# Kernel optimization log

Hardware: AMD Instinct MI355X
Metric: run time of the kernel (lower is better)

## Reference

```python
import jax, jax.numpy as jnp
import numpy as np

K = 4          # knn (loop=True -> self included as nearest)
NEG_SLOPE = 0.2  # PyG GATConv leaky_relu slope


def knn_neighbors(coords, k=K):
    """coords: [B, P, 2] -> global neighbor indices [B*P, k].
    Per-batch brute-force kNN (cdist + top_k), sequential over batch to
    bound the [P, P] distance matrix memory, matching torch_cluster.knn_graph
    with loop=True and a per-image batch vector."""
    B, P, _ = coords.shape

    def per_batch(c):  # c: [P, 2]
        d = jnp.sum((c[:, None, :] - c[None, :, :]) ** 2, axis=-1)  # [P, P]
        _, idx = jax.lax.top_k(-d, k)  # self (dist 0) is included -> loop=True
        return idx

    idx = jax.lax.map(per_batch, coords)  # [B, P, k], local indices
    offs = (jnp.arange(B, dtype=idx.dtype) * P)[:, None, None]
    return (idx + offs).reshape(B * P, k)  # global node ids


def gat_layer(x, nbr, W, a_src, a_dst, b, concat):
    """PyG GATConv (eval mode, dropout off) on a fixed-degree kNN graph.
    x: [N, Cin], nbr: [N, k] source nodes j for each target i.
    alpha_ij = softmax_j leaky_relu(a_src.h_j + a_dst.h_i); out_i = sum_j alpha_ij h_j."""
    H, F = a_src.shape
    h = (x @ W).reshape(-1, H, F)                      # [N, H, F]
    asrc = jnp.einsum('nhf,hf->nh', h, a_src)          # [N, H]
    adst = jnp.einsum('nhf,hf->nh', h, a_dst)          # [N, H]
    e = jax.nn.leaky_relu(asrc[nbr] + adst[:, None, :], NEG_SLOPE)  # [N, k, H]
    alpha = jax.nn.softmax(e, axis=1)                  # softmax over neighbors
    out = jnp.einsum('nkh,nkhf->nhf', alpha, h[nbr])   # [N, H, F]
    if concat:
        out = out.reshape(-1, H * F)
    else:
        out = out.mean(axis=1)                         # heads=1 -> identity
    return out + b


def gat_forward(coords, x, W0, att_src0, att_dst0, b0, W1, att_src1, att_dst1, b1,
                W2, att_src2, att_dst2, b2):
    B, P, _ = coords.shape
    nbr = knn_neighbors(coords)
    h = gat_layer(x, nbr, W0, att_src0, att_dst0, b0, concat=True)
    h = jax.nn.elu(h)
    h = gat_layer(h, nbr, W1, att_src1, att_dst1, b1, concat=True)
    h = jax.nn.elu(h)
    h = gat_layer(h, nbr, W2, att_src2, att_dst2, b2, concat=False)
    return h.reshape(B, P, -1)  # pred_logits [B, P, num_classes+1]


def setup_inputs() -> dict:
    key = jax.random.key(0)
    ks = jax.random.split(key, 16)
    B, P, N = 16, 8192, 16 * 8192
    s = 0.05
    return {
        'coords': jax.random.uniform(ks[0], (B, P, 2), dtype=jnp.float32),
        'x': jax.random.normal(ks[1], (N, 256), dtype=jnp.float32),
        'W0': jax.random.normal(ks[2], (256, 256), dtype=jnp.float32) * s,
        'att_src0': jax.random.normal(ks[3], (4, 64), dtype=jnp.float32) * s,
        'att_dst0': jax.random.normal(ks[4], (4, 64), dtype=jnp.float32) * s,
        'b0': jax.random.normal(ks[5], (256,), dtype=jnp.float32) * s,
        'W1': jax.random.normal(ks[6], (256, 256), dtype=jnp.float32) * s,
        'att_src1': jax.random.normal(ks[7], (4, 64), dtype=jnp.float32) * s,
        'att_dst1': jax.random.normal(ks[8], (4, 64), dtype=jnp.float32) * s,
        'b1': jax.random.normal(ks[9], (256,), dtype=jnp.float32) * s,
        'W2': jax.random.normal(ks[10], (256, 2), dtype=jnp.float32) * s,
        'att_src2': jax.random.normal(ks[11], (1, 2), dtype=jnp.float32) * s,
        'att_dst2': jax.random.normal(ks[12], (1, 2), dtype=jnp.float32) * s,
        'b2': jax.random.normal(ks[13], (2,), dtype=jnp.float32) * s,
    }


def reference(coords, x, W0, att_src0, att_dst0, b0, W1, att_src1, att_dst1, b1,
              W2, att_src2, att_dst2, b2):
    return gat_forward(coords, x, W0, att_src0, att_dst0, b0,
                       W1, att_src1, att_dst1, b1, W2, att_src2, att_dst2, b2)
```

## Files before the change

### kernel.cpp

```cpp
#include <hip/hip_runtime.h>
#include <math.h>

constexpr int Bn = 16, Pn = 8192, Nn = 16 * 8192;
constexpr int GB = 32;
constexpr int NBIN = GB * GB;

typedef __attribute__((ext_vector_type(8))) short short8;
typedef __attribute__((ext_vector_type(4))) float f32x4;

__device__ __forceinline__ unsigned short f2bf(float f) {
  unsigned u = __builtin_bit_cast(unsigned, f);
  unsigned r = (u + 0x7FFFu + ((u >> 16) & 1u)) >> 16;
  return (unsigned short)r;
}
__device__ __forceinline__ float bf2f(unsigned short h) {
  unsigned u = ((unsigned)h) << 16;
  return __builtin_bit_cast(float, u);
}

__global__ __launch_bounds__(256) void bin_count(const float* __restrict__ coords,
                                                 int* __restrict__ counts) {
  const int n = blockIdx.x * 256 + threadIdx.x;
  const int b = n >> 13;
  float2 c = ((const float2*)coords)[n];
  int bx = min(GB - 1, (int)(c.x * (float)GB));
  int by = min(GB - 1, (int)(c.y * (float)GB));
  atomicAdd(&counts[b * NBIN + by * GB + bx], 1);
}

__global__ __launch_bounds__(1024) void bin_scan(const int* __restrict__ counts,
                                                 int* __restrict__ starts,
                                                 int* __restrict__ cursor) {
  __shared__ int s[NBIN];
  const int b = blockIdx.x, t = threadIdx.x;
  const int v = counts[b * NBIN + t];
  s[t] = v;
  __syncthreads();
  for (int off = 1; off < NBIN; off <<= 1) {
    int x = (t >= off) ? s[t - off] : 0;
    __syncthreads();
    s[t] += x;
    __syncthreads();
  }
  const int excl = s[t] - v;
  starts[b * NBIN + t] = excl;
  cursor[b * NBIN + t] = excl;
}

__global__ __launch_bounds__(256) void bin_scatter(const float* __restrict__ coords,
                                                   int* __restrict__ cursor,
                                                   float2* __restrict__ pts,
                                                   int* __restrict__ ids) {
  const int n = blockIdx.x * 256 + threadIdx.x;
  const int b = n >> 13, p = n & (Pn - 1);
  float2 c = ((const float2*)coords)[n];
  int bx = min(GB - 1, (int)(c.x * (float)GB));
  int by = min(GB - 1, (int)(c.y * (float)GB));
  int slot = atomicAdd(&cursor[b * NBIN + by * GB + bx], 1);
  pts[(size_t)b * Pn + slot] = c;
  ids[(size_t)b * Pn + slot] = p;
}

__global__ __launch_bounds__(256) void knn_query(const float* __restrict__ coords,
                                                 const int* __restrict__ starts,
                                                 const int* __restrict__ counts,
                                                 const float2* __restrict__ pts,
                                                 const int* __restrict__ ids,
                                                 int* __restrict__ nbr) {
  const int n = blockIdx.x * 256 + threadIdx.x;
  const int b = n >> 13;
  const float2 q = ((const float2*)coords)[n];
  const float qx = q.x, qy = q.y;
  const float w = 1.0f / (float)GB;
  const int bx = min(GB - 1, (int)(qx * (float)GB));
  const int by = min(GB - 1, (int)(qy * (float)GB));
  const float2* bp = pts + (size_t)b * Pn;
  const int* bi = ids + (size_t)b * Pn;
  const int* bs = starts + b * NBIN;
  const int* bc = counts + b * NBIN;

  float d0v = 3.4e38f, d1v = 3.4e38f, d2v = 3.4e38f, d3v = 3.4e38f;
  int i0v = 0x7fffffff, i1v = 0x7fffffff, i2v = 0x7fffffff, i3v = 0x7fffffff;

#define LLT(da, ia, db, ib) ((da) < (db) || ((da) == (db) && (ia) < (ib)))
#define LEX_INSERT(dd, jj)                                              \
  if (LLT(dd, jj, d3v, i3v)) {                                          \
    if (LLT(dd, jj, d2v, i2v)) {                                        \
      d3v = d2v; i3v = i2v;                                             \
      if (LLT(dd, jj, d1v, i1v)) {                                      \
        d2v = d1v; i2v = i1v;                                           \
        if (LLT(dd, jj, d0v, i0v)) { d1v = d0v; i1v = i0v; d0v = dd; i0v = jj; } \
        else { d1v = dd; i1v = jj; }                                    \
      } else { d2v = dd; i2v = jj; }                                    \
    } else { d3v = dd; i3v = jj; }                                      \
  }
#define SCAN_CELL(xx, yy)                                               \
  {                                                                     \
    const int cell = (yy) * GB + (xx);                                  \
    const int s0 = bs[cell], cnt = bc[cell];                            \
    for (int s = s0; s < s0 + cnt; ++s) {                               \
      float2 pp = bp[s];                                                \
      int jj = bi[s];                                                   \
      float dx = qx - pp.x, dy = qy - pp.y;                             \
      float dd = __fadd_rn(__fmul_rn(dx, dx), __fmul_rn(dy, dy));       \
      LEX_INSERT(dd, jj);                                               \
    }                                                                   \
  }

  for (int k = 0; k < GB; ++k) {
    const int xlo = bx - k, xhi = bx + k, ylo = by - k, yhi = by + k;
    const int cxlo = max(0, xlo), cxhi = min(GB - 1, xhi);
    const int cylo = max(0, ylo), cyhi = min(GB - 1, yhi);
    for (int yy = cylo; yy <= cyhi; ++yy) {
      const bool edge = (yy == ylo) || (yy == yhi);
      if (edge || k == 0) {
        for (int xx = cxlo; xx <= cxhi; ++xx) SCAN_CELL(xx, yy);
      } else {
        if (xlo >= 0) SCAN_CELL(xlo, yy);
        if (xhi <= GB - 1) SCAN_CELL(xhi, yy);
      }
    }
    float m = 1e30f;
    bool open = false;
    if (xlo > 0)      { m = fminf(m, qx - (float)xlo * w); open = true; }
    if (xhi < GB - 1) { m = fminf(m, (float)(xhi + 1) * w - qx); open = true; }
    if (ylo > 0)      { m = fminf(m, qy - (float)ylo * w); open = true; }
    if (yhi < GB - 1) { m = fminf(m, (float)(yhi + 1) * w - qy); open = true; }
    if (!open) break;
    m -= 1e-6f;
    if (d3v < 3.0e38f && m > 0.f && __fmul_rn(m, m) >= d3v) break;
  }
#undef SCAN_CELL
#undef LEX_INSERT
#undef LLT

  const int base = b * Pn;
  *(int4*)&nbr[(size_t)n * 4] =
      make_int4(base + i0v, base + i1v, base + i2v, base + i3v);
}

__global__ __launch_bounds__(256) void wt_kernel(const float* __restrict__ W,
                                                 unsigned short* __restrict__ Wth,
                                                 unsigned short* __restrict__ Wtl) {
  const int k = blockIdx.x, n = threadIdx.x;
  float v = W[k * 256 + n];
  unsigned short h = f2bf(v);
  unsigned short l = f2bf(v - bf2f(h));
  Wth[n * 256 + k] = h;
  Wtl[n * 256 + k] = l;
}

__global__ __launch_bounds__(256, 3) void gemm_bf3(const float* __restrict__ A,
                                                   const unsigned short* __restrict__ Bth,
                                                   const unsigned short* __restrict__ Btl,
                                                   const float* __restrict__ att_src,
                                                   const float* __restrict__ att_dst,
                                                   float* __restrict__ C,
                                                   float* __restrict__ asrc,
                                                   float* __restrict__ adst) {
  __shared__ unsigned short Ah[128][36], Al[128][36];
  __shared__ unsigned short Bh[128][36], Bl[128][36];
  const int t = threadIdx.x;
  const int row0 = blockIdx.y * 128;
  const int col0 = blockIdx.x * 128;
  const int wid = t >> 6, lane = t & 63;
  const int wr = (wid >> 1) * 64, wc = (wid & 1) * 64;
  const int lrow = lane & 15, lko = (lane >> 4) * 8;

  f32x4 acc[4][4];
#pragma unroll
  for (int i = 0; i < 4; ++i)
#pragma unroll
    for (int j = 0; j < 4; ++j) acc[i][j] = {0.f, 0.f, 0.f, 0.f};

  float4 av[4];
  uint4 bhv[2], blv[2];

#define GLOAD(ktv)                                                          \
  {                                                                         \
    const int k0 = (ktv) * 32;                                              \
    _Pragma("unroll")                                                       \
    for (int i = 0; i < 4; ++i) {                                           \
      const int idx = t + i * 256;                                          \
      const int row = idx >> 3, kq = idx & 7;                               \
      av[i] = *(const float4*)&A[(size_t)(row0 + row) * 256 + k0 + kq * 4]; \
    }                                                                       \
    _Pragma("unroll")                                                       \
    for (int i = 0; i < 2; ++i) {                                           \
      const int idx = t + i * 256;                                          \
      const int col = idx >> 2, kc = idx & 3;                               \
      bhv[i] = *(const uint4*)&Bth[(size_t)(col0 + col) * 256 + k0 + kc * 8]; \
      blv[i] = *(const uint4*)&Btl[(size_t)(col0 + col) * 256 + k0 + kc * 8]; \
    }                                                                       \
  }

  GLOAD(0);
  for (int kt = 0; kt < 8; ++kt) {
    __syncthreads();
#pragma unroll
    for (int i = 0; i < 4; ++i) {
      const int idx = t + i * 256;
      const int row = idx >> 3, kq = idx & 7;
      const float vv[4] = {av[i].x, av[i].y, av[i].z, av[i].w};
      unsigned short hh[4], ll[4];
#pragma unroll
      for (int e = 0; e < 4; ++e) {
        hh[e] = f2bf(vv[e]);
        ll[e] = f2bf(vv[e] - bf2f(hh[e]));
      }
      *(ushort4*)&Ah[row][kq * 4] = make_ushort4(hh[0], hh[1], hh[2], hh[3]);
      *(ushort4*)&Al[row][kq * 4] = make_ushort4(ll[0], ll[1], ll[2], ll[3]);
    }
#pragma unroll
    for (int i = 0; i < 2; ++i) {
      const int idx = t + i * 256;
      const int col = idx >> 2, kc = idx & 3;
      *(uint4*)&Bh[col][kc * 8] = bhv[i];
      *(uint4*)&Bl[col][kc * 8] = blv[i];
    }
    __syncthreads();
    if (kt < 7) GLOAD(kt + 1);
    short8 afh[4], afl[4], bfh[4], bfl[4];
#pragma unroll
    for (int f = 0; f < 4; ++f) {
      afh[f] = *(const short8*)&Ah[wr + f * 16 + lrow][lko];
      afl[f] = *(const short8*)&Al[wr + f * 16 + lrow][lko];
      bfh[f] = *(const short8*)&Bh[wc + f * 16 + lrow][lko];
      bfl[f] = *(const short8*)&Bl[wc + f * 16 + lrow][lko];
    }
#pragma unroll
    for (int fr = 0; fr < 4; ++fr)
#pragma unroll
      for (int fc = 0; fc < 4; ++fc) {
        acc[fr][fc] = __builtin_amdgcn_mfma_f32_16x16x32_bf16(afh[fr], bfh[fc], acc[fr][fc], 0, 0, 0);
        acc[fr][fc] = __builtin_amdgcn_mfma_f32_16x16x32_bf16(afh[fr], bfl[fc], acc[fr][fc], 0, 0, 0);
        acc[fr][fc] = __builtin_amdgcn_mfma_f32_16x16x32_bf16(afl[fr], bfh[fc], acc[fr][fc], 0, 0, 0);
      }
  }
#undef GLOAD

#pragma unroll
  for (int fr = 0; fr < 4; ++fr)
#pragma unroll
    for (int fc = 0; fc < 4; ++fc) {
      const int col = col0 + wc + fc * 16 + lrow;
#pragma unroll
      for (int j = 0; j < 4; ++j) {
        const int row = row0 + wr + fr * 16 + (lane >> 4) * 4 + j;
        C[(size_t)row * 256 + col] = acc[fr][fc][j];
      }
    }

  const int h = (col0 >> 6) + (wid & 1);
  float asv[4], adv[4];
#pragma unroll
  for (int fc = 0; fc < 4; ++fc) {
    asv[fc] = att_src[h * 64 + fc * 16 + lrow];
    adv[fc] = att_dst[h * 64 + fc * 16 + lrow];
  }
#pragma unroll
  for (int fr = 0; fr < 4; ++fr)
#pragma unroll
    for (int j = 0; j < 4; ++j) {
      float ps = 0.f, pd = 0.f;
#pragma unroll
      for (int fc = 0; fc < 4; ++fc) {
        ps += acc[fr][fc][j] * asv[fc];
        pd += acc[fr][fc][j] * adv[fc];
      }
#pragma unroll
      for (int off = 1; off < 16; off <<= 1) {
        ps += __shfl_xor(ps, off);
        pd += __shfl_xor(pd, off);
      }
      if (lrow == 0) {
        const int row = row0 + wr + fr * 16 + (lane >> 4) * 4 + j;
        asrc[(size_t)row * 4 + h] = ps;
        adst[(size_t)row * 4 + h] = pd;
      }
    }
}

__device__ __forceinline__ float leaky02(float x) { return x >= 0.f ? x : 0.2f * x; }

__global__ __launch_bounds__(256) void aggregate_fused(const float* __restrict__ g,
                                                       const int* __restrict__ nbr,
                                                       const float* __restrict__ asrc,
                                                       const float* __restrict__ adst,
                                                       const float* __restrict__ bias,
                                                       float* __restrict__ y) {
  const int t = threadIdx.x;
  const int lane = t & 63;
  const int n = blockIdx.x * 4 + (t >> 6);
  int4 nb = *(const int4*)&nbr[(size_t)n * 4];
  const int h = lane >> 4;
  const float adh = adst[(size_t)n * 4 + h];
  float e0 = leaky02(asrc[(size_t)nb.x * 4 + h] + adh);
  float e1 = leaky02(asrc[(size_t)nb.y * 4 + h] + adh);
  float e2 = leaky02(asrc[(size_t)nb.z * 4 + h] + adh);
  float e3 = leaky02(asrc[(size_t)nb.w * 4 + h] + adh);
  float m = fmaxf(fmaxf(fmaxf(e0, e1), e2), e3);
  float x0 = expf(e0 - m), x1 = expf(e1 - m), x2 = expf(e2 - m), x3 = expf(e3 - m);
  float s = ((x0 + x1) + x2) + x3;
  const float a0 = x0 / s, a1 = x1 / s, a2 = x2 / s, a3 = x3 / s;

  const int c = lane * 4;
  float4 v0 = *(const float4*)&g[(size_t)nb.x * 256 + c];
  float4 v1 = *(const float4*)&g[(size_t)nb.y * 256 + c];
  float4 v2 = *(const float4*)&g[(size_t)nb.z * 256 + c];
  float4 v3 = *(const float4*)&g[(size_t)nb.w * 256 + c];
  float4 bb = *(const float4*)&bias[c];
  float4 o;
  o.x = a0 * v0.x + a1 * v1.x + a2 * v2.x + a3 * v3.x + bb.x;
  o.y = a0 * v0.y + a1 * v1.y + a2 * v2.y + a3 * v3.y + bb.y;
  o.z = a0 * v0.z + a1 * v1.z + a2 * v2.z + a3 * v3.z + bb.z;
  o.w = a0 * v0.w + a1 * v1.w + a2 * v2.w + a3 * v3.w + bb.w;
  o.x = o.x > 0.f ? o.x : expm1f(o.x);
  o.y = o.y > 0.f ? o.y : expm1f(o.y);
  o.z = o.z > 0.f ? o.z : expm1f(o.z);
  o.w = o.w > 0.f ? o.w : expm1f(o.w);
  *(float4*)&y[(size_t)n * 256 + c] = o;
}

__global__ __launch_bounds__(256) void aggregate_h2(const float* __restrict__ g,
                                                    const int* __restrict__ nbr,
                                                    const float* __restrict__ asrc,
                                                    const float* __restrict__ adst,
                                                    const float* __restrict__ bias,
                                                    const float* __restrict__ W2,
                                                    const float* __restrict__ as2,
                                                    const float* __restrict__ ad2,
                                                    float* __restrict__ g2,
                                                    float* __restrict__ asrc2,
                                                    float* __restrict__ adst2) {
  const int t = threadIdx.x;
  const int lane = t & 63;
  const int n = blockIdx.x * 4 + (t >> 6);
  int4 nb = *(const int4*)&nbr[(size_t)n * 4];
  const int h = lane >> 4;
  const float adh = adst[(size_t)n * 4 + h];
  float e0 = leaky02(asrc[(size_t)nb.x * 4 + h] + adh);
  float e1 = leaky02(asrc[(size_t)nb.y * 4 + h] + adh);
  float e2 = leaky02(asrc[(size_t)nb.z * 4 + h] + adh);
  float e3 = leaky02(asrc[(size_t)nb.w * 4 + h] + adh);
  float m = fmaxf(fmaxf(fmaxf(e0, e1), e2), e3);
  float x0 = expf(e0 - m), x1 = expf(e1 - m), x2 = expf(e2 - m), x3 = expf(e3 - m);
  float s = ((x0 + x1) + x2) + x3;
  const float a0 = x0 / s, a1 = x1 / s, a2 = x2 / s, a3 = x3 / s;

  const int c = lane * 4;
  float4 v0 = *(const float4*)&g[(size_t)nb.x * 256 + c];
  float4 v1 = *(const float4*)&g[(size_t)nb.y * 256 + c];
  float4 v2 = *(const float4*)&g[(size_t)nb.z * 256 + c];
  float4 v3 = *(const float4*)&g[(size_t)nb.w * 256 + c];
  float4 bb = *(const float4*)&bias[c];
  float4 o;
  o.x = a0 * v0.x + a1 * v1.x + a2 * v2.x + a3 * v3.x + bb.x;
  o.y = a0 * v0.y + a1 * v1.y + a2 * v2.y + a3 * v3.y + bb.y;
  o.z = a0 * v0.z + a1 * v1.z + a2 * v2.z + a3 * v3.z + bb.z;
  o.w = a0 * v0.w + a1 * v1.w + a2 * v2.w + a3 * v3.w + bb.w;
  o.x = o.x > 0.f ? o.x : expm1f(o.x);
  o.y = o.y > 0.f ? o.y : expm1f(o.y);
  o.z = o.z > 0.f ? o.z : expm1f(o.z);
  o.w = o.w > 0.f ? o.w : expm1f(o.w);

  const float w00 = W2[(c + 0) * 2 + 0], w01 = W2[(c + 0) * 2 + 1];
  const float w10 = W2[(c + 1) * 2 + 0], w11 = W2[(c + 1) * 2 + 1];
  const float w20 = W2[(c + 2) * 2 + 0], w21 = W2[(c + 2) * 2 + 1];
  const float w30 = W2[(c + 3) * 2 + 0], w31 = W2[(c + 3) * 2 + 1];
  float p0 = o.x * w00 + o.y * w10 + o.z * w20 + o.w * w30;
  float p1 = o.x * w01 + o.y * w11 + o.z * w21 + o.w * w31;
#pragma unroll
  for (int off = 1; off < 64; off <<= 1) {
    p0 += __shfl_xor(p0, off);
    p1 += __shfl_xor(p1, off);
  }
  if (lane == 0) {
    g2[(size_t)n * 2]     = p0;
    g2[(size_t)n * 2 + 1] = p1;
    asrc2[n] = p0 * as2[0] + p1 * as2[1];
    adst2[n] = p0 * ad2[0] + p1 * ad2[1];
  }
}

__global__ __launch_bounds__(256) void final_kernel(const int* __restrict__ nbr,
                                                    const float* __restrict__ g2,
                                                    const float* __restrict__ asrc2,
                                                    const float* __restrict__ adst2,
                                                    const float* __restrict__ b2,
                                                    float* __restrict__ out) {
  const int n = blockIdx.x * 256 + threadIdx.x;
  int4 nb = *(const int4*)&nbr[(size_t)n * 4];
  const float ad = adst2[n];
  float e0 = leaky02(asrc2[nb.x] + ad);
  float e1 = leaky02(asrc2[nb.y] + ad);
  float e2 = leaky02(asrc2[nb.z] + ad);
  float e3 = leaky02(asrc2[nb.w] + ad);
  float m = fmaxf(fmaxf(e0, e1), fmaxf(e2, e3));
  float x0 = expf(e0 - m), x1 = expf(e1 - m), x2 = expf(e2 - m), x3 = expf(e3 - m);
  float s = x0 + x1 + x2 + x3;
  float o0 = (x0 * g2[(size_t)nb.x * 2] + x1 * g2[(size_t)nb.y * 2] +
              x2 * g2[(size_t)nb.z * 2] + x3 * g2[(size_t)nb.w * 2]) / s;
  float o1 = (x0 * g2[(size_t)nb.x * 2 + 1] + x1 * g2[(size_t)nb.y * 2 + 1] +
              x2 * g2[(size_t)nb.z * 2 + 1] + x3 * g2[(size_t)nb.w * 2 + 1]) / s;
  out[(size_t)n * 2]     = o0 + b2[0];
  out[(size_t)n * 2 + 1] = o1 + b2[1];
}

extern "C" void kernel_launch(void* const* d_in, const int* in_sizes, int n_in,
                              void* d_out, int out_size, void* d_ws, size_t ws_size,
                              hipStream_t stream) {
  const float* coords = (const float*)d_in[0];
  const float* x   = (const float*)d_in[1];
  const float* W0  = (const float*)d_in[2];
  const float* as0 = (const float*)d_in[3];
  const float* ad0 = (const float*)d_in[4];
  const float* b0  = (const float*)d_in[5];
  const float* W1  = (const float*)d_in[6];
  const float* as1 = (const float*)d_in[7];
  const float* ad1 = (const float*)d_in[8];
  const float* b1  = (const float*)d_in[9];
  const float* W2  = (const float*)d_in[10];
  const float* as2 = (const float*)d_in[11];
  const float* ad2 = (const float*)d_in[12];
  const float* b2  = (const float*)d_in[13];
  float* out = (float*)d_out;

  float* g     = (float*)d_ws;
  float* y     = g + (size_t)Nn * 256;
  int*   nbr   = (int*)(y + (size_t)Nn * 256);
  float* asrc  = (float*)(nbr + (size_t)Nn * 4);
  float* adst  = asrc + (size_t)Nn * 4;
  float* g2    = adst + (size_t)Nn * 4;
  float* s2    = g2 + (size_t)Nn * 2;
  float* d2    = s2 + (size_t)Nn;
  unsigned short* Wth = (unsigned short*)(d2 + (size_t)Nn);
  unsigned short* Wtl = Wth + 256 * 256;
  float2* pts  = (float2*)(Wtl + 256 * 256);
  int* ids     = (int*)(pts + (size_t)Bn * Pn);
  int* counts  = ids + (size_t)Bn * Pn;
  int* starts  = counts + Bn * NBIN;
  int* cursor  = starts + Bn * NBIN;

  hipMemsetAsync(counts, 0, Bn * NBIN * sizeof(int), stream);
  bin_count<<<Nn / 256, 256, 0, stream>>>(coords, counts);
  bin_scan<<<Bn, NBIN, 0, stream>>>(counts, starts, cursor);
  bin_scatter<<<Nn / 256, 256, 0, stream>>>(coords, cursor, pts, ids);
  knn_query<<<Nn / 256, 256, 0, stream>>>(coords, starts, counts, pts, ids, nbr);

  wt_kernel<<<256, 256, 0, stream>>>(W0, Wth, Wtl);
  gemm_bf3<<<dim3(2, Nn / 128), 256, 0, stream>>>(x, Wth, Wtl, as0, ad0, g, asrc, adst);
  aggregate_fused<<<Nn / 4, 256, 0, stream>>>(g, nbr, asrc, adst, b0, y);

  wt_kernel<<<256, 256, 0, stream>>>(W1, Wth, Wtl);
  gemm_bf3<<<dim3(2, Nn / 128), 256, 0, stream>>>(y, Wth, Wtl, as1, ad1, g, asrc, adst);
  aggregate_h2<<<Nn / 4, 256, 0, stream>>>(g, nbr, asrc, adst, b1, W2, as2, ad2,
                                           g2, s2, d2);

  final_kernel<<<Nn / 256, 256, 0, stream>>>(nbr, g2, s2, d2, b2, out);
}
```

Before: 706.7 us.

## Load GEMM B fragments directly from global and swap MFMA operands for vector stores

The pre-split bf16 weight fragments are now read straight from global memory (L2/L1-resident) into registers instead of being staged through shared memory. This halves the LDS footprint and the LDS traffic per k-step. The MFMA operands are swapped so each lane holds 4 consecutive output columns, which allows float4 stores of C and an attention-logit reduction needing only two cross-lane shuffles instead of four. The cost is more global load instructions per wave, each issued right before its use with little latency hiding.

```diff
diff --git a/kernel.cpp b/kernel.cpp
--- a/kernel.cpp
+++ b/kernel.cpp
@@ -159,13 +159,13 @@
                                                    float* __restrict__ asrc,
                                                    float* __restrict__ adst) {
   __shared__ unsigned short Ah[128][36], Al[128][36];
-  __shared__ unsigned short Bh[128][36], Bl[128][36];
   const int t = threadIdx.x;
   const int row0 = blockIdx.y * 128;
   const int col0 = blockIdx.x * 128;
   const int wid = t >> 6, lane = t & 63;
   const int wr = (wid >> 1) * 64, wc = (wid & 1) * 64;
   const int lrow = lane & 15, lko = (lane >> 4) * 8;
+  const int cg = (lane >> 4) * 4;
 
   f32x4 acc[4][4];
 #pragma unroll
@@ -174,7 +174,6 @@
     for (int j = 0; j < 4; ++j) acc[i][j] = {0.f, 0.f, 0.f, 0.f};
 
   float4 av[4];
-  uint4 bhv[2], blv[2];
 
 #define GLOAD(ktv)                                                          \
   {                                                                         \
@@ -185,13 +184,6 @@
       const int row = idx >> 3, kq = idx & 7;                               \
       av[i] = *(const float4*)&A[(size_t)(row0 + row) * 256 + k0 + kq * 4]; \
     }                                                                       \
-    _Pragma("unroll")                                                       \
-    for (int i = 0; i < 2; ++i) {                                           \
-      const int idx = t + i * 256;                                          \
-      const int col = idx >> 2, kc = idx & 3;                               \
-      bhv[i] = *(const uint4*)&Bth[(size_t)(col0 + col) * 256 + k0 + kc * 8]; \
-      blv[i] = *(const uint4*)&Btl[(size_t)(col0 + col) * 256 + k0 + kc * 8]; \
-    }                                                                       \
   }
 
   GLOAD(0);
@@ -211,74 +203,68 @@
       *(ushort4*)&Ah[row][kq * 4] = make_ushort4(hh[0], hh[1], hh[2], hh[3]);
       *(ushort4*)&Al[row][kq * 4] = make_ushort4(ll[0], ll[1], ll[2], ll[3]);
     }
-#pragma unroll
-    for (int i = 0; i < 2; ++i) {
-      const int idx = t + i * 256;
-      const int col = idx >> 2, kc = idx & 3;
-      *(uint4*)&Bh[col][kc * 8] = bhv[i];
-      *(uint4*)&Bl[col][kc * 8] = blv[i];
-    }
     __syncthreads();
     if (kt < 7) GLOAD(kt + 1);
-    short8 afh[4], afl[4], bfh[4], bfl[4];
+
+    short8 bfh[4], bfl[4];
+#pragma unroll
+    for (int f = 0; f < 4; ++f) {
+      const size_t boff = (size_t)(col0 + wc + f * 16 + lrow) * 256 + kt * 32 + lko;
+      bfh[f] = *(const short8*)&Bth[boff];
+      bfl[f] = *(const short8*)&Btl[boff];
+    }
+    short8 afh[4], afl[4];
 #pragma unroll
     for (int f = 0; f < 4; ++f) {
       afh[f] = *(const short8*)&Ah[wr + f * 16 + lrow][lko];
       afl[f] = *(const short8*)&Al[wr + f * 16 + lrow][lko];
-      bfh[f] = *(const short8*)&Bh[wc + f * 16 + lrow][lko];
-      bfl[f] = *(const short8*)&Bl[wc + f * 16 + lrow][lko];
     }
 #pragma unroll
     for (int fr = 0; fr < 4; ++fr)
 #pragma unroll
       for (int fc = 0; fc < 4; ++fc) {
-        acc[fr][fc] = __builtin_amdgcn_mfma_f32_16x16x32_bf16(afh[fr], bfh[fc], acc[fr][fc], 0, 0, 0);
-        acc[fr][fc] = __builtin_amdgcn_mfma_f32_16x16x32_bf16(afh[fr], bfl[fc], acc[fr][fc], 0, 0, 0);
-        acc[fr][fc] = __builtin_amdgcn_mfma_f32_16x16x32_bf16(afl[fr], bfh[fc], acc[fr][fc], 0, 0, 0);
+        acc[fr][fc] = __builtin_amdgcn_mfma_f32_16x16x32_bf16(bfh[fc], afh[fr], acc[fr][fc], 0, 0, 0);
+        acc[fr][fc] = __builtin_amdgcn_mfma_f32_16x16x32_bf16(bfl[fc], afh[fr], acc[fr][fc], 0, 0, 0);
+        acc[fr][fc] = __builtin_amdgcn_mfma_f32_16x16x32_bf16(bfh[fc], afl[fr], acc[fr][fc], 0, 0, 0);
       }
   }
 #undef GLOAD
 
 #pragma unroll
-  for (int fr = 0; fr < 4; ++fr)
+  for (int fr = 0; fr < 4; ++fr) {
+    const int row = row0 + wr + fr * 16 + lrow;
 #pragma unroll
     for (int fc = 0; fc < 4; ++fc) {
-      const int col = col0 + wc + fc * 16 + lrow;
-#pragma unroll
-      for (int j = 0; j < 4; ++j) {
-        const int row = row0 + wr + fr * 16 + (lane >> 4) * 4 + j;
-        C[(size_t)row * 256 + col] = acc[fr][fc][j];
-      }
-    }
+      const int col = col0 + wc + fc * 16 + cg;
+      *(f32x4*)&C[(size_t)row * 256 + col] = acc[fr][fc];
+    }
+  }
 
   const int h = (col0 >> 6) + (wid & 1);
-  float asv[4], adv[4];
+  float4 asv[4], adv[4];
 #pragma unroll
   for (int fc = 0; fc < 4; ++fc) {
-    asv[fc] = att_src[h * 64 + fc * 16 + lrow];
-    adv[fc] = att_dst[h * 64 + fc * 16 + lrow];
-  }
-#pragma unroll
-  for (int fr = 0; fr < 4; ++fr)
-#pragma unroll
-    for (int j = 0; j < 4; ++j) {
-      float ps = 0.f, pd = 0.f;
-#pragma unroll
-      for (int fc = 0; fc < 4; ++fc) {
-        ps += acc[fr][fc][j] * asv[fc];
-        pd += acc[fr][fc][j] * adv[fc];
-      }
-#pragma unroll
-      for (int off = 1; off < 16; off <<= 1) {
-        ps += __shfl_xor(ps, off);
-        pd += __shfl_xor(pd, off);
-      }
-      if (lrow == 0) {
-        const int row = row0 + wr + fr * 16 + (lane >> 4) * 4 + j;
-        asrc[(size_t)row * 4 + h] = ps;
-        adst[(size_t)row * 4 + h] = pd;
-      }
-    }
+    asv[fc] = *(const float4*)&att_src[h * 64 + fc * 16 + cg];
+    adv[fc] = *(const float4*)&att_dst[h * 64 + fc * 16 + cg];
+  }
+#pragma unroll
+  for (int fr = 0; fr < 4; ++fr) {
+    float ps = 0.f, pd = 0.f;
+#pragma unroll
+    for (int fc = 0; fc < 4; ++fc) {
+      ps += acc[fr][fc][0] * asv[fc].x + acc[fr][fc][1] * asv[fc].y +
+            acc[fr][fc][2] * asv[fc].z + acc[fr][fc][3] * asv[fc].w;
+      pd += acc[fr][fc][0] * adv[fc].x + acc[fr][fc][1] * adv[fc].y +
+            acc[fr][fc][2] * adv[fc].z + acc[fr][fc][3] * adv[fc].w;
+    }
+    ps += __shfl_xor(ps, 16); ps += __shfl_xor(ps, 32);
+    pd += __shfl_xor(pd, 16); pd += __shfl_xor(pd, 32);
+    if (lane < 16) {
+      const int row = row0 + wr + fr * 16 + lrow;
+      asrc[(size_t)row * 4 + h] = ps;
+      adst[(size_t)row * 4 + h] = pd;
+    }
+  }
 }
 
 __device__ __forceinline__ float leaky02(float x) { return x >= 0.f ? x : 0.2f * x; }
```

After: 635.4 us. -10.1%, faster.
